# Kernel tuning notes

Measured on AMD Instinct MI355X. Metric: run time of the kernel, lower is better.

The kernel has to match this reference:

```python
import jax, jax.numpy as jnp
import numpy as np

M, N, L, D = 2048, 256, 128, 300  # context len, n entities, query len, d2
DROOT = float(np.sqrt(D))


def setup_inputs() -> dict:
    key = jax.random.key(0)
    ks = jax.random.split(key, 16)
    s = 0.05
    return {
        "context_emb": jax.random.normal(ks[0], (M, D), jnp.float32),
        "query_emb": jax.random.normal(ks[1], (L, D), jnp.float32),
        "bin_M": (jax.random.uniform(ks[2], (M, N)) < 0.02).astype(jnp.float32),  # sparse token->entity incidence
        "adj": (jax.random.uniform(ks[3], (N, N)) < 0.05).astype(jnp.float32),    # entity graph adjacency
        "V": jax.random.normal(ks[4], (D, 2 * D), jnp.float32) * s,
        "U": jax.random.normal(ks[5], (D, 2 * D), jnp.float32) * s,
        "b": jax.random.normal(ks[6], (D,), jnp.float32) * s,
        "W": jax.random.normal(ks[7], (2 * D,), jnp.float32) * s,
        "w_att": jax.random.normal(ks[8], (3, D), jnp.float32) * s,   # BiDAF trilinear weights (w_c, w_q, w_cq)
        "b_att": jax.random.normal(ks[9], (3,), jnp.float32) * s,
        "W_red": jax.random.normal(ks[10], (D, 4 * D), jnp.float32) * s,  # BiDAF reduction Linear(4*d2 -> d2)
        "b_red": jax.random.normal(ks[11], (D,), jnp.float32) * s,
        "W_ih": jax.random.normal(ks[12], (4 * D, 2 * D), jnp.float32) * s,  # LSTM input weights
        "b_ih": jax.random.normal(ks[13], (4 * D,), jnp.float32) * s,
        "b_hh": jax.random.normal(ks[14], (4 * D,), jnp.float32) * s,
        "passes": 1,
    }


def _tok2ent(context, bin_M):
    # avg_pool1d over full M divides by M (zeros of unmasked tokens included) -> exact mean/M
    mean = (bin_M.T @ context) / M                       # (N, D)
    masked = context[:, None, :] * bin_M[:, :, None]     # (M, N, D) dominant intermediate
    mx = masked.max(axis=0)                              # (N, D) max includes the zeros, as in torch
    return jnp.concatenate([mean, mx], axis=-1)          # (N, 2D)


def _graph_attention(ent, query, adj, V, U, b, W):
    q = query.mean(axis=0)                               # avg-pooled query (D,)
    gammas = ((q @ V) @ ent.T) / DROOT                   # (N,)
    E = jax.nn.sigmoid(gammas)[:, None] * ent            # soft entity mask, (N, 2D)
    hidden = E @ U.T + b                                 # (N, D)
    a_i = hidden @ W[:D]                                 # (N,) source half of W.[h_i;h_j]
    c_j = hidden @ W[D:]                                 # (N,)
    betas = jnp.where(adj > 0, jax.nn.leaky_relu(a_i[:, None] + c_j[None, :]), 0.0)
    # original exponentiates ALL betas incl. the zeros of non-edges -> plain softmax over axis 1
    alphas = jax.nn.softmax(betas, axis=1)               # (N, N)
    # E_t[i] = relu( sum_{j: adj[i,j]} alphas[j,i] * hidden[j] )
    return jax.nn.relu((adj * alphas.T) @ hidden)        # (N, D)


def _bidaf(ent, query, w_att, b_att, W_red, b_red):
    # trilinear similarity S[l, n] = w_c.q_l + w_q.e_n + w_cq.(q_l * e_n)
    S = (query @ w_att[0] + b_att[0])[:, None] \
        + (ent @ w_att[1] + b_att[1])[None, :] \
        + (query * w_att[2]) @ ent.T + b_att[2]          # (L, N)
    c2q = jax.nn.softmax(S, axis=1) @ ent                # (L, D)
    q2c = jax.nn.softmax(S.max(axis=1), axis=0) @ query  # (D,)
    x = jnp.concatenate([query, c2q, query * c2q, query * q2c[None, :]], axis=-1)  # (L, 4D)
    return x @ W_red.T + b_red                           # (L, D)


def _graph2doc(context, ent, bin_M, W_ih, b_ih, b_hh):
    x = jnp.concatenate([context, bin_M @ ent], axis=-1)  # (M, 2D)
    # nn.LSTM fed (seq=1, batch=M, 2D) from zero state == one LSTM-cell step per token
    gates = x @ W_ih.T + (b_ih + b_hh)                    # (M, 4D), torch gate order i,f,g,o
    i, f, g, o = jnp.split(gates, 4, axis=-1)
    c = jax.nn.sigmoid(i) * jnp.tanh(g)                   # f*c0 vanishes since c0 = 0
    return jax.nn.sigmoid(o) * jnp.tanh(c)                # (M, D)


def reference(context_emb, query_emb, bin_M, adj, V, U, b, W, w_att, b_att,
              W_red, b_red, W_ih, b_ih, b_hh, passes):
    ctx, qry = context_emb, query_emb
    for _ in range(passes):
        ent = _tok2ent(ctx, bin_M)                        # (N, 2D)
        E_t = _graph_attention(ent, qry, adj, V, U, b, W)  # (N, D)
        qry = _bidaf(E_t, qry, w_att, b_att, W_red, b_red)  # (L, D)
        ctx = _graph2doc(ctx, E_t, bin_M, W_ih, b_ih, b_hh)  # (M, D)
    return ctx, qry
```

## Files before the change

### kernel.cpp

```cpp
#include <hip/hip_runtime.h>
#include <hip/hip_bf16.h>
#include <math.h>

#define MM 2048
#define NN 256
#define LL 128
#define DD 300
#define D2 600
#define D4 1200
#define DROOT 17.320508075688775f

#define KP 608
#define NP 960
#define GM 64
#define GDT 64
#define GK 32

typedef __attribute__((ext_vector_type(8))) short bf16x8;
typedef __attribute__((ext_vector_type(4))) float f32x4;

__device__ __forceinline__ float sigmoidf_(float x) { return 1.f / (1.f + expf(-x)); }

__device__ __forceinline__ ushort f2bf(float v) {
    union { float f; unsigned u; } x; x.f = v;
    unsigned r = x.u + 0x7fffu + ((x.u >> 16) & 1u);
    return (ushort)(r >> 16);
}

__device__ __forceinline__ float dot4_(float4 a, float4 b) {
    return a.x * b.x + a.y * b.y + a.z * b.z + a.w * b.w;
}

__device__ __forceinline__ float bfdot8(uint4 u, float4 x0, float4 x1) {
    union { unsigned v; float f; } a, b;
    float s = 0.f;
    a.v = u.x << 16; b.v = u.x & 0xffff0000u; s += a.f * x0.x; s += b.f * x0.y;
    a.v = u.y << 16; b.v = u.y & 0xffff0000u; s += a.f * x0.z; s += b.f * x0.w;
    a.v = u.z << 16; b.v = u.z & 0xffff0000u; s += a.f * x1.x; s += b.f * x1.y;
    a.v = u.w << 16; b.v = u.w & 0xffff0000u; s += a.f * x1.z; s += b.f * x1.w;
    return s;
}

__device__ __forceinline__ float wave_red_sum(float v) {
    for (int off = 32; off; off >>= 1) v += __shfl_down(v, off);
    return v;
}

__global__ __launch_bounds__(256) void k_prep(const float* __restrict__ binM,
                                              const float* __restrict__ Wih,
                                              const float* __restrict__ U,
                                              const float* __restrict__ Wred,
                                              const float* __restrict__ query,
                                              const float* __restrict__ V,
                                              ushort* __restrict__ Wb,
                                              ushort* __restrict__ Ub,
                                              ushort* __restrict__ Wredb,
                                              unsigned* __restrict__ binMbits,
                                              float* __restrict__ qVp) {
    __shared__ float qp2[2][75];
    __shared__ float qp_s[75];
    int r = blockIdx.x, t = threadIdx.x;
    if (r < 12) {
        int kb = r >> 2, sl = r & 3;
        int dbase = sl * 75;
        if (t < 150) {
            int dd = t % 75, half = t / 75;
            float s = 0.f;
            #pragma unroll 8
            for (int l = half * 64; l < half * 64 + 64; ++l) s += query[l * DD + dbase + dd];
            qp2[half][dd] = s;
        }
        __syncthreads();
        if (t < 75) qp_s[t] = (qp2[0][t] + qp2[1][t]) * (1.f / LL);
        __syncthreads();
        int k = kb * 256 + t;
        if (k < D2) {
            float acc = 0.f;
            #pragma unroll 5
            for (int i = 0; i < 75; ++i) acc += qp_s[i] * V[(size_t)(dbase + i) * D2 + k];
            qVp[sl * D2 + k] = acc;
        }
    } else if (r < 76) {
        int blk = r - 12;
        int m0 = blk * 32;
        unsigned mask = 0u;
        #pragma unroll 8
        for (int i = 0; i < 32; ++i) {
            if (binM[(size_t)(m0 + i) * NN + t] != 0.f) mask |= (1u << i);
        }
        binMbits[(size_t)t * 64 + blk] = mask;
    } else if (r < 76 + NP) {
        int rr = r - 76;
        int s = rr / 320, dd = rr % 320;
        bool valid = (dd < DD);
        int src = (s == 0) ? dd : ((s == 1) ? 600 + dd : 900 + dd);
        for (int e = t; e < KP; e += 256) {
            float v = (valid && e < D2) ? Wih[(size_t)src * D2 + e] : 0.f;
            Wb[(size_t)rr * KP + e] = f2bf(v);
        }
    } else if (r < 76 + NP + DD) {
        int rr = r - 76 - NP;
        for (int e = t; e < D2; e += 256) Ub[(size_t)rr * D2 + e] = f2bf(U[(size_t)rr * D2 + e]);
    } else {
        int rr = r - 76 - NP - DD;
        for (int e = t; e < D4; e += 256) Wredb[(size_t)rr * D4 + e] = f2bf(Wred[(size_t)rr * D4 + e]);
    }
}

__global__ __launch_bounds__(960) void k_hidden(const float* __restrict__ ctx,
                                                const unsigned* __restrict__ binMbits,
                                                const float* __restrict__ qVp,
                                                const ushort* __restrict__ Ub,
                                                const float* __restrict__ bvec,
                                                const float* __restrict__ W,
                                                float* __restrict__ hidden,
                                                float* __restrict__ a_i,
                                                float* __restrict__ c_j) {
    __shared__ int lst[MM];
    __shared__ int wbase_s[65];
    __shared__ alignas(16) float e_s[D2];
    __shared__ float h_s[DD];
    __shared__ float red[2][16];
    __shared__ float sig_s;
    int n = blockIdx.x, t = threadIdx.x, wv = t >> 6, lane = t & 63;
    unsigned mword = (t < 64) ? binMbits[(size_t)n * 64 + t] : 0u;
    if (t < 64) wbase_s[t] = (int)__popc(mword);
    __syncthreads();
    if (t == 0) {
        int s = 0;
        for (int w = 0; w < 64; ++w) { int c = wbase_s[w]; wbase_s[w] = s; s += c; }
        wbase_s[64] = s;
    }
    __syncthreads();
    if (t < 64) {
        int base = wbase_s[t];
        unsigned x = mword;
        while (x) {
            int b = __ffs((int)x) - 1;
            lst[base++] = t * 32 + b;
            x &= x - 1;
        }
    }
    __syncthreads();
    int total = wbase_s[64];
    if (t < DD) {
        float sum = 0.f, mx = 0.f;
        int i = 0;
        for (; i + 4 <= total; i += 4) {
            float v0 = ctx[(size_t)lst[i] * DD + t];
            float v1 = ctx[(size_t)lst[i + 1] * DD + t];
            float v2 = ctx[(size_t)lst[i + 2] * DD + t];
            float v3 = ctx[(size_t)lst[i + 3] * DD + t];
            sum += v0; mx = fmaxf(mx, v0);
            sum += v1; mx = fmaxf(mx, v1);
            sum += v2; mx = fmaxf(mx, v2);
            sum += v3; mx = fmaxf(mx, v3);
        }
        for (; i < total; ++i) {
            float v = ctx[(size_t)lst[i] * DD + t];
            sum += v; mx = fmaxf(mx, v);
        }
        e_s[t]      = sum * (1.f / MM);
        e_s[DD + t] = mx;
    }
    __syncthreads();
    float part = 0.f;
    if (t < D2) part = e_s[t] * (qVp[t] + qVp[D2 + t] + qVp[2 * D2 + t] + qVp[3 * D2 + t]);
    part = wave_red_sum(part);
    if (lane == 0) red[0][wv] = part;
    __syncthreads();
    if (t == 0) {
        float s = 0.f;
        for (int w = 0; w < 15; ++w) s += red[0][w];
        sig_s = sigmoidf_(s / DROOT);
    }
    __syncthreads();
    float sg = sig_s;
    const float4* e4 = (const float4*)e_s;
    float4 ex0 = e4[2 * lane], ex1 = e4[2 * lane + 1];
    float4 ex2 = {0.f, 0.f, 0.f, 0.f}, ex3 = {0.f, 0.f, 0.f, 0.f};
    if (lane < 11) { ex2 = e4[128 + 2 * lane]; ex3 = e4[129 + 2 * lane]; }
    #pragma unroll 4
    for (int i = 0; i < 20; ++i) {
        int d = wv * 20 + i;
        const uint4* u4 = (const uint4*)(Ub + (size_t)d * D2);
        float p2 = bfdot8(u4[lane], ex0, ex1);
        if (lane < 11) p2 += bfdot8(u4[64 + lane], ex2, ex3);
        p2 = wave_red_sum(p2);
        if (lane == 0) {
            float h = sg * p2 + bvec[d];
            h_s[d] = h;
            hidden[n * DD + d] = h;
        }
    }
    __syncthreads();
    float wa = 0.f, wc = 0.f;
    if (t < DD) { float h = h_s[t]; wa = h * W[t]; wc = h * W[DD + t]; }
    wa = wave_red_sum(wa); wc = wave_red_sum(wc);
    if (lane == 0) { red[0][wv] = wa; red[1][wv] = wc; }
    __syncthreads();
    if (t == 0) {
        float A = 0.f, C = 0.f;
        for (int w = 0; w < 15; ++w) { A += red[0][w]; C += red[1][w]; }
        a_i[n] = A; c_j[n] = C;
    }
}

__global__ __launch_bounds__(256) void k_alphas(const float* __restrict__ adj,
                                                const float* __restrict__ ai,
                                                const float* __restrict__ cj,
                                                float* __restrict__ alphas) {
    __shared__ float red[4];
    __shared__ float bc[2];
    int i = blockIdx.x, j = threadIdx.x;
    float beta = 0.f;
    if (adj[i * NN + j] > 0.f) {
        float v = ai[i] + cj[j];
        beta = (v > 0.f) ? v : 0.01f * v;
    }
    float wm = beta;
    for (int off = 32; off; off >>= 1) wm = fmaxf(wm, __shfl_down(wm, off));
    if ((j & 63) == 0) red[j >> 6] = wm;
    __syncthreads();
    if (j == 0) bc[0] = fmaxf(fmaxf(red[0], red[1]), fmaxf(red[2], red[3]));
    __syncthreads();
    float e = expf(beta - bc[0]);
    float ws_ = e;
    for (int off = 32; off; off >>= 1) ws_ += __shfl_down(ws_, off);
    __syncthreads();
    if ((j & 63) == 0) red[j >> 6] = ws_;
    __syncthreads();
    if (j == 0) bc[1] = 1.f / (red[0] + red[1] + red[2] + red[3]);
    __syncthreads();
    alphas[i * NN + j] = e * bc[1];
}

__global__ __launch_bounds__(960) void k_Et(const float* __restrict__ adj,
                                            const float* __restrict__ alphas,
                                            const float* __restrict__ hidden,
                                            const float* __restrict__ w_att,
                                            const float* __restrict__ b_att,
                                            float* __restrict__ Et,
                                            float* __restrict__ EtT,
                                            float* __restrict__ ce) {
    __shared__ float w_s[NN];
    __shared__ float epart[3][DD];
    __shared__ float red[16];
    int i = blockIdx.x, t = threadIdx.x, wv = t >> 6;
    if (t < NN) w_s[t] = adj[i * NN + t] * alphas[t * NN + i];
    __syncthreads();
    int d = t % 320, sl = t / 320;
    int j0 = sl * 86, j1 = (sl == 2) ? NN : (j0 + 86);
    if (d < DD) {
        float acc = 0.f;
        #pragma unroll 2
        for (int j = j0; j < j1; ++j) acc += w_s[j] * hidden[(size_t)j * DD + d];
        epart[sl][d] = acc;
    }
    __syncthreads();
    float pv = 0.f;
    if (t < DD) {
        float etv = fmaxf(epart[0][t] + epart[1][t] + epart[2][t], 0.f);
        Et[i * DD + t] = etv;
        EtT[(size_t)t * NN + i] = etv;
        pv = etv * w_att[DD + t];
    }
    pv = wave_red_sum(pv);
    if ((t & 63) == 0) red[wv] = pv;
    __syncthreads();
    if (t == 0) {
        float s = 0.f;
        for (int w = 0; w < 15; ++w) s += red[w];
        ce[i] = s + b_att[1];
    }
}

__global__ __launch_bounds__(1024) void k_Bmid(const float* __restrict__ query,
                                               const float* __restrict__ Et,
                                               const float* __restrict__ EtT,
                                               const float* __restrict__ w_att,
                                               const float* __restrict__ b_att,
                                               const float* __restrict__ ce,
                                               const float* __restrict__ ctx,
                                               const float* __restrict__ binM,
                                               float* __restrict__ rowmax,
                                               float* __restrict__ c2qg,
                                               ushort* __restrict__ Xb) {
    __shared__ alignas(16) float qw[DD];
    __shared__ float s_row[NN];
    __shared__ alignas(16) float p_s[NN];
    __shared__ float red[16];
    __shared__ float cql_s, rmax_s, invs;
    __shared__ int lst4[4][NN];
    __shared__ int wcnt4[4][4];
    __shared__ int tot4[4];
    int t = threadIdx.x, wv = t >> 6, lane = t & 63;
    if (blockIdx.x < MM / 4) {
        int g = t >> 8, tt = t & 255;
        int w2 = tt >> 6;
        int m = blockIdx.x * 4 + g;
        float b = binM[(size_t)m * NN + tt];
        unsigned long long mask = __ballot(b != 0.f);
        int prefix = __popcll(mask & ((1ull << lane) - 1ull));
        if (lane == 0) wcnt4[g][w2] = (int)__popcll(mask);
        __syncthreads();
        int wbase = 0;
        for (int w = 0; w < w2; ++w) wbase += wcnt4[g][w];
        if (b != 0.f) lst4[g][wbase + prefix] = tt;
        if (tt == 0) tot4[g] = wcnt4[g][0] + wcnt4[g][1] + wcnt4[g][2] + wcnt4[g][3];
        __syncthreads();
        int total = tot4[g];
        if (tt < 8) Xb[(size_t)m * KP + D2 + tt] = 0;
        for (int d = tt; d < DD; d += 256) {
            Xb[(size_t)m * KP + d] = f2bf(ctx[(size_t)m * DD + d]);
            float s = 0.f;
            for (int i = 0; i < total; ++i) s += Et[(size_t)lst4[g][i] * DD + d];
            Xb[(size_t)m * KP + DD + d] = f2bf(s);
        }
    } else {
        int l = blockIdx.x - MM / 4;
        float part = 0.f;
        if (t < DD) {
            float qv = query[l * DD + t];
            qw[t] = qv * w_att[2 * DD + t];
            part = qv * w_att[t];
        }
        part = wave_red_sum(part);
        if (lane == 0) red[wv] = part;
        __syncthreads();
        if (t == 0) {
            float s = 0.f;
            for (int w = 0; w < 16; ++w) s += red[w];
            cql_s = s + b_att[0];
        }
        __syncthreads();
        const float4* q4 = (const float4*)qw;
        float4 qb0 = q4[lane];
        float4 qb1 = (lane < 11) ? q4[64 + lane] : float4{0.f, 0.f, 0.f, 0.f};
        float wmax = -1e30f;
        #pragma unroll 4
        for (int i = 0; i < 16; ++i) {
            int n = wv * 16 + i;
            const float4* e4 = (const float4*)(Et + (size_t)n * DD);
            float4 a0 = e4[lane];
            float p2 = dot4_(a0, qb0);
            if (lane < 11) { float4 a1 = e4[64 + lane]; p2 += dot4_(a1, qb1); }
            p2 = wave_red_sum(p2);
            if (lane == 0) {
                float val = cql_s + ce[n] + p2 + b_att[2];
                s_row[n] = val;
                wmax = fmaxf(wmax, val);
            }
        }
        if (lane == 0) red[wv] = wmax;
        __syncthreads();
        if (t == 0) {
            float m = red[0];
            for (int w = 1; w < 16; ++w) m = fmaxf(m, red[w]);
            rmax_s = m;
            rowmax[l] = m;
        }
        __syncthreads();
        float e = 0.f;
        if (t < NN) e = expf(s_row[t] - rmax_s);
        float v = wave_red_sum(e);
        if (lane == 0) red[wv] = v;
        __syncthreads();
        if (t == 0) {
            float s = 0.f;
            for (int w = 0; w < 16; ++w) s += red[w];
            invs = 1.f / s;
        }
        __syncthreads();
        if (t < NN) p_s[t] = e * invs;
        __syncthreads();
        if (wv < 15) {
            const float4* p4 = (const float4*)p_s;
            float4 pb = p4[lane];
            #pragma unroll 4
            for (int i = 0; i < 20; ++i) {
                int d = wv * 20 + i;
                float4 a = ((const float4*)(EtT + (size_t)d * NN))[lane];
                float p2 = wave_red_sum(dot4_(a, pb));
                if (lane == 0) c2qg[l * DD + d] = p2;
            }
        }
    }
}

__global__ __launch_bounds__(320) void k_tail(const float* __restrict__ c2qg,
                                              const float* __restrict__ rowmax,
                                              const float* __restrict__ query,
                                              const ushort* __restrict__ Wredb,
                                              const float* __restrict__ bred,
                                              const ushort* __restrict__ Xb,
                                              const ushort* __restrict__ Wb,
                                              const float* __restrict__ bih,
                                              const float* __restrict__ bhh,
                                              float* __restrict__ outq,
                                              float* __restrict__ outc) {
    __shared__ float pq[LL];
    __shared__ float q2c_s[DD];
    __shared__ alignas(16) float xs[D4];
    __shared__ float red[5];
    __shared__ float bc2[2];
    __shared__ ushort As[GM * GK];
    __shared__ ushort Bs[3][GDT * GK];
    int t = threadIdx.x, wv = t >> 6, lane = t & 63;
    if (blockIdx.x < 160) {
        int g = blockIdx.x;
        int m0 = (g & 31) * GM, d0 = (g >> 5) * GDT;
        int tid = t;
        int wm = wv >> 1, wn = wv & 1;
        int l15 = lane & 15, l4 = lane >> 4;
        f32x4 acc[3][2][2] = {};
        int srow = tid >> 2, kslot = tid & 3;
        int sidx = srow * GK + ((kslot ^ ((srow >> 1) & 3)) << 3);
        for (int k0 = 0; k0 < KP; k0 += GK) {
            if (tid < 256) {
                uint4 va = *(const uint4*)(Xb + (size_t)(m0 + srow) * KP + k0 + kslot * 8);
                *(uint4*)(As + sidx) = va;
                #pragma unroll
                for (int s = 0; s < 3; ++s) {
                    uint4 vb = *(const uint4*)(Wb + (size_t)(s * 320 + d0 + srow) * KP + k0 + kslot * 8);
                    *(uint4*)(Bs[s] + sidx) = vb;
                }
            }
            __syncthreads();
            if (tid < 256) {
                bf16x8 af[2], bfr[3][2];
                #pragma unroll
                for (int mi = 0; mi < 2; ++mi) {
                    int row = wm * 32 + mi * 16 + l15;
                    af[mi] = *(const bf16x8*)(As + row * GK + ((l4 ^ ((row >> 1) & 3)) << 3));
                }
                #pragma unroll
                for (int s = 0; s < 3; ++s)
                    #pragma unroll
                    for (int ni = 0; ni < 2; ++ni) {
                        int row = wn * 32 + ni * 16 + l15;
                        bfr[s][ni] = *(const bf16x8*)(Bs[s] + row * GK + ((l4 ^ ((row >> 1) & 3)) << 3));
                    }
                #pragma unroll
                for (int s = 0; s < 3; ++s)
                    #pragma unroll
                    for (int mi = 0; mi < 2; ++mi)
                        #pragma unroll
                        for (int ni = 0; ni < 2; ++ni)
                            acc[s][mi][ni] = __builtin_amdgcn_mfma_f32_16x16x32_bf16(af[mi], bfr[s][ni], acc[s][mi][ni], 0, 0, 0);
            }
            __syncthreads();
        }
        if (tid < 256) {
            #pragma unroll
            for (int mi = 0; mi < 2; ++mi) {
                #pragma unroll
                for (int ni = 0; ni < 2; ++ni) {
                    int d = d0 + wn * 32 + ni * 16 + l15;
                    if (d < DD) {
                        float bi = bih[d] + bhh[d];
                        float bg = bih[2 * DD + d] + bhh[2 * DD + d];
                        float bo = bih[3 * DD + d] + bhh[3 * DD + d];
                        int mrow = m0 + wm * 32 + mi * 16 + l4 * 4;
                        #pragma unroll
                        for (int r2 = 0; r2 < 4; ++r2) {
                            float gi = acc[0][mi][ni][r2] + bi;
                            float gg = acc[1][mi][ni][r2] + bg;
                            float go = acc[2][mi][ni][r2] + bo;
                            float c = sigmoidf_(gi) * tanhf(gg);
                            outc[(size_t)(mrow + r2) * DD + d] = sigmoidf_(go) * tanhf(c);
                        }
                    }
                }
            }
        }
    } else {
        int idx = blockIdx.x - 160;
        int s = idx / LL, l = idx % LL;
        float v = (t < LL) ? rowmax[t] : -1e30f;
        float wm = v;
        for (int off = 32; off; off >>= 1) wm = fmaxf(wm, __shfl_down(wm, off));
        if (lane == 0) red[wv] = wm;
        __syncthreads();
        if (t == 0) {
            float m = red[0];
            for (int w = 1; w < 5; ++w) m = fmaxf(m, red[w]);
            bc2[0] = m;
        }
        __syncthreads();
        float e = (t < LL) ? expf(v - bc2[0]) : 0.f;
        float ws_ = wave_red_sum(e);
        __syncthreads();
        if (lane == 0) red[wv] = ws_;
        __syncthreads();
        if (t == 0) {
            float sm = 0.f;
            for (int w = 0; w < 5; ++w) sm += red[w];
            bc2[1] = 1.f / sm;
        }
        __syncthreads();
        if (t < LL) pq[t] = e * bc2[1];
        __syncthreads();
        if (t < DD) {
            float s2 = 0.f;
            #pragma unroll 4
            for (int l2 = 0; l2 < LL; ++l2) s2 += pq[l2] * query[l2 * DD + t];
            q2c_s[t] = s2;
        }
        __syncthreads();
        if (t < DD) {
            float c = c2qg[l * DD + t];
            float qv = query[l * DD + t];
            xs[t] = qv; xs[DD + t] = c; xs[2 * DD + t] = qv * c; xs[3 * DD + t] = qv * q2c_s[t];
        }
        __syncthreads();
        const float4* x4 = (const float4*)xs;
        float4 xb0 = x4[2 * lane], xb1 = x4[2 * lane + 1];
        float4 xb2 = x4[128 + 2 * lane], xb3 = x4[129 + 2 * lane];
        float4 xb4 = {0.f, 0.f, 0.f, 0.f}, xb5 = {0.f, 0.f, 0.f, 0.f};
        if (lane < 22) { xb4 = x4[256 + 2 * lane]; xb5 = x4[257 + 2 * lane]; }
        int d0 = s * 100 + wv * 20;
        #pragma unroll 2
        for (int i = 0; i < 20; ++i) {
            int d = d0 + i;
            const uint4* w4 = (const uint4*)(Wredb + (size_t)d * D4);
            float p2 = bfdot8(w4[lane], xb0, xb1) + bfdot8(w4[64 + lane], xb2, xb3);
            if (lane < 22) p2 += bfdot8(w4[128 + lane], xb4, xb5);
            p2 = wave_red_sum(p2);
            if (lane == 0) outq[l * DD + d] = bred[d] + p2;
        }
    }
}

extern "C" void kernel_launch(void* const* d_in, const int* in_sizes, int n_in,
                              void* d_out, int out_size, void* d_ws, size_t ws_size,
                              hipStream_t stream) {
    const float* context = (const float*)d_in[0];
    const float* query   = (const float*)d_in[1];
    const float* binM    = (const float*)d_in[2];
    const float* adj     = (const float*)d_in[3];
    const float* V       = (const float*)d_in[4];
    const float* U       = (const float*)d_in[5];
    const float* bvec    = (const float*)d_in[6];
    const float* W       = (const float*)d_in[7];
    const float* w_att   = (const float*)d_in[8];
    const float* b_att   = (const float*)d_in[9];
    const float* W_red   = (const float*)d_in[10];
    const float* b_red   = (const float*)d_in[11];
    const float* W_ih    = (const float*)d_in[12];
    const float* b_ih    = (const float*)d_in[13];
    const float* b_hh    = (const float*)d_in[14];

    float* ws = (float*)d_ws;
    float* qVp    = ws;
    float* hidden = qVp    + 2400;
    float* a_i    = hidden + 76800;
    float* c_j    = a_i    + 256;
    float* alphas = c_j    + 256;
    float* Et     = alphas + 65536;
    float* EtT    = Et     + 76800;
    float* ce     = EtT    + 76800;
    float* rmax   = ce     + 256;
    float* c2qg   = rmax   + 128;
    unsigned* binMbits = (unsigned*)(c2qg + 38400);
    ushort* Xb    = (ushort*)(binMbits + (size_t)NN * 64);
    ushort* Wb    = Xb + (size_t)MM * KP;
    ushort* Ub    = Wb + (size_t)NP * KP;
    ushort* Wredb = Ub + (size_t)DD * D2;

    float* outc = (float*)d_out;
    float* outq = (float*)d_out + MM * DD;

    hipLaunchKernelGGL(k_prep,    dim3(76 + NP + 2 * DD), dim3(256), 0, stream,
                       binM, W_ih, U, W_red, query, V, Wb, Ub, Wredb, binMbits, qVp);
    hipLaunchKernelGGL(k_hidden,  dim3(NN), dim3(960), 0, stream, context, binMbits, qVp, Ub, bvec, W, hidden, a_i, c_j);
    hipLaunchKernelGGL(k_alphas,  dim3(NN), dim3(256), 0, stream, adj, a_i, c_j, alphas);
    hipLaunchKernelGGL(k_Et,      dim3(NN), dim3(960), 0, stream, adj, alphas, hidden, w_att, b_att, Et, EtT, ce);
    hipLaunchKernelGGL(k_Bmid,    dim3(MM / 4 + LL), dim3(1024), 0, stream,
                       query, Et, EtT, w_att, b_att, ce, context, binM, rmax, c2qg, Xb);
    hipLaunchKernelGGL(k_tail,    dim3(160 + 3 * LL), dim3(320), 0, stream,
                       c2qg, rmax, query, Wredb, b_red, Xb, Wb, b_ih, b_hh, outq, outc);
}
```

Measured before the change: 116.9 us.

## Fuse hidden, alphas and Et kernels into one cooperative kernel with grid syncs

Merges the three graph-attention kernels into a single cooperative launch that uses grid.sync between phases, removing two kernel launch boundaries. The alphas phase now stores only per-row max and inverse sum, and the Et phase recomputes each softmax weight on the fly, so the 256x256 alphas matrix is no longer written or read. In exchange it adds cooperative-launch overhead and grid-wide barriers, and requires all 256 blocks of 960 threads to be co-resident.

Measured after the change: 174.0 us. +48.8%, slower.

```diff
diff --git a/kernel.cpp b/kernel.cpp
--- a/kernel.cpp
+++ b/kernel.cpp
@@ -1,6 +1,9 @@
 #include <hip/hip_runtime.h>
+#include <hip/hip_cooperative_groups.h>
 #include <hip/hip_bf16.h>
 #include <math.h>
+
+namespace cg = cooperative_groups;
 
 #define MM 2048
 #define NN 256
@@ -107,171 +110,184 @@
     }
 }
 
-__global__ __launch_bounds__(960) void k_hidden(const float* __restrict__ ctx,
-                                                const unsigned* __restrict__ binMbits,
-                                                const float* __restrict__ qVp,
-                                                const ushort* __restrict__ Ub,
-                                                const float* __restrict__ bvec,
-                                                const float* __restrict__ W,
-                                                float* __restrict__ hidden,
-                                                float* __restrict__ a_i,
-                                                float* __restrict__ c_j) {
+__global__ __launch_bounds__(960) void k_mid(const float* __restrict__ ctx,
+                                             const unsigned* __restrict__ binMbits,
+                                             const float* __restrict__ qVp,
+                                             const ushort* __restrict__ Ub,
+                                             const float* __restrict__ adj,
+                                             const float* __restrict__ bvec,
+                                             const float* __restrict__ W,
+                                             const float* __restrict__ w_att,
+                                             const float* __restrict__ b_att,
+                                             float* __restrict__ hidden,
+                                             float* __restrict__ a_i,
+                                             float* __restrict__ c_j,
+                                             float* __restrict__ mstat,
+                                             float* __restrict__ rinv,
+                                             float* __restrict__ Et,
+                                             float* __restrict__ EtT,
+                                             float* __restrict__ ce) {
+    cg::grid_group grid = cg::this_grid();
     __shared__ int lst[MM];
     __shared__ int wbase_s[65];
     __shared__ alignas(16) float e_s[D2];
     __shared__ float h_s[DD];
     __shared__ float red[2][16];
-    __shared__ float sig_s;
-    int n = blockIdx.x, t = threadIdx.x, wv = t >> 6, lane = t & 63;
-    unsigned mword = (t < 64) ? binMbits[(size_t)n * 64 + t] : 0u;
-    if (t < 64) wbase_s[t] = (int)__popc(mword);
-    __syncthreads();
-    if (t == 0) {
-        int s = 0;
-        for (int w = 0; w < 64; ++w) { int c = wbase_s[w]; wbase_s[w] = s; s += c; }
-        wbase_s[64] = s;
-    }
-    __syncthreads();
-    if (t < 64) {
-        int base = wbase_s[t];
-        unsigned x = mword;
-        while (x) {
-            int b = __ffs((int)x) - 1;
-            lst[base++] = t * 32 + b;
-            x &= x - 1;
-        }
-    }
-    __syncthreads();
-    int total = wbase_s[64];
-    if (t < DD) {
-        float sum = 0.f, mx = 0.f;
-        int i = 0;
-        for (; i + 4 <= total; i += 4) {
-            float v0 = ctx[(size_t)lst[i] * DD + t];
-            float v1 = ctx[(size_t)lst[i + 1] * DD + t];
-            float v2 = ctx[(size_t)lst[i + 2] * DD + t];
-            float v3 = ctx[(size_t)lst[i + 3] * DD + t];
-            sum += v0; mx = fmaxf(mx, v0);
-            sum += v1; mx = fmaxf(mx, v1);
-            sum += v2; mx = fmaxf(mx, v2);
-            sum += v3; mx = fmaxf(mx, v3);
-        }
-        for (; i < total; ++i) {
-            float v = ctx[(size_t)lst[i] * DD + t];
-            sum += v; mx = fmaxf(mx, v);
-        }
-        e_s[t]      = sum * (1.f / MM);
-        e_s[DD + t] = mx;
-    }
-    __syncthreads();
-    float part = 0.f;
-    if (t < D2) part = e_s[t] * (qVp[t] + qVp[D2 + t] + qVp[2 * D2 + t] + qVp[3 * D2 + t]);
-    part = wave_red_sum(part);
-    if (lane == 0) red[0][wv] = part;
-    __syncthreads();
-    if (t == 0) {
-        float s = 0.f;
-        for (int w = 0; w < 15; ++w) s += red[0][w];
-        sig_s = sigmoidf_(s / DROOT);
-    }
-    __syncthreads();
-    float sg = sig_s;
-    const float4* e4 = (const float4*)e_s;
-    float4 ex0 = e4[2 * lane], ex1 = e4[2 * lane + 1];
-    float4 ex2 = {0.f, 0.f, 0.f, 0.f}, ex3 = {0.f, 0.f, 0.f, 0.f};
-    if (lane < 11) { ex2 = e4[128 + 2 * lane]; ex3 = e4[129 + 2 * lane]; }
-    #pragma unroll 4
-    for (int i = 0; i < 20; ++i) {
-        int d = wv * 20 + i;
-        const uint4* u4 = (const uint4*)(Ub + (size_t)d * D2);
-        float p2 = bfdot8(u4[lane], ex0, ex1);
-        if (lane < 11) p2 += bfdot8(u4[64 + lane], ex2, ex3);
-        p2 = wave_red_sum(p2);
-        if (lane == 0) {
-            float h = sg * p2 + bvec[d];
-            h_s[d] = h;
-            hidden[n * DD + d] = h;
-        }
-    }
-    __syncthreads();
-    float wa = 0.f, wc = 0.f;
-    if (t < DD) { float h = h_s[t]; wa = h * W[t]; wc = h * W[DD + t]; }
-    wa = wave_red_sum(wa); wc = wave_red_sum(wc);
-    if (lane == 0) { red[0][wv] = wa; red[1][wv] = wc; }
-    __syncthreads();
-    if (t == 0) {
-        float A = 0.f, C = 0.f;
-        for (int w = 0; w < 15; ++w) { A += red[0][w]; C += red[1][w]; }
-        a_i[n] = A; c_j[n] = C;
-    }
-}
-
-__global__ __launch_bounds__(256) void k_alphas(const float* __restrict__ adj,
-                                                const float* __restrict__ ai,
-                                                const float* __restrict__ cj,
-                                                float* __restrict__ alphas) {
-    __shared__ float red[4];
-    __shared__ float bc[2];
-    int i = blockIdx.x, j = threadIdx.x;
-    float beta = 0.f;
-    if (adj[i * NN + j] > 0.f) {
-        float v = ai[i] + cj[j];
-        beta = (v > 0.f) ? v : 0.01f * v;
-    }
-    float wm = beta;
-    for (int off = 32; off; off >>= 1) wm = fmaxf(wm, __shfl_down(wm, off));
-    if ((j & 63) == 0) red[j >> 6] = wm;
-    __syncthreads();
-    if (j == 0) bc[0] = fmaxf(fmaxf(red[0], red[1]), fmaxf(red[2], red[3]));
-    __syncthreads();
-    float e = expf(beta - bc[0]);
-    float ws_ = e;
-    for (int off = 32; off; off >>= 1) ws_ += __shfl_down(ws_, off);
-    __syncthreads();
-    if ((j & 63) == 0) red[j >> 6] = ws_;
-    __syncthreads();
-    if (j == 0) bc[1] = 1.f / (red[0] + red[1] + red[2] + red[3]);
-    __syncthreads();
-    alphas[i * NN + j] = e * bc[1];
-}
-
-__global__ __launch_bounds__(960) void k_Et(const float* __restrict__ adj,
-                                            const float* __restrict__ alphas,
-                                            const float* __restrict__ hidden,
-                                            const float* __restrict__ w_att,
-                                            const float* __restrict__ b_att,
-                                            float* __restrict__ Et,
-                                            float* __restrict__ EtT,
-                                            float* __restrict__ ce) {
+    __shared__ float scal[2];
     __shared__ float w_s[NN];
     __shared__ float epart[3][DD];
-    __shared__ float red[16];
-    int i = blockIdx.x, t = threadIdx.x, wv = t >> 6;
-    if (t < NN) w_s[t] = adj[i * NN + t] * alphas[t * NN + i];
-    __syncthreads();
-    int d = t % 320, sl = t / 320;
-    int j0 = sl * 86, j1 = (sl == 2) ? NN : (j0 + 86);
-    if (d < DD) {
-        float acc = 0.f;
-        #pragma unroll 2
-        for (int j = j0; j < j1; ++j) acc += w_s[j] * hidden[(size_t)j * DD + d];
-        epart[sl][d] = acc;
+    int bid = blockIdx.x, t = threadIdx.x, wv = t >> 6, lane = t & 63;
+
+    {
+        int n = bid;
+        unsigned mword = (t < 64) ? binMbits[(size_t)n * 64 + t] : 0u;
+        if (t < 64) wbase_s[t] = (int)__popc(mword);
+        __syncthreads();
+        if (t == 0) {
+            int s = 0;
+            for (int w = 0; w < 64; ++w) { int c = wbase_s[w]; wbase_s[w] = s; s += c; }
+            wbase_s[64] = s;
+        }
+        __syncthreads();
+        if (t < 64) {
+            int base = wbase_s[t];
+            unsigned x = mword;
+            while (x) {
+                int b = __ffs((int)x) - 1;
+                lst[base++] = t * 32 + b;
+                x &= x - 1;
+            }
+        }
+        __syncthreads();
+        int total = wbase_s[64];
+        if (t < DD) {
+            float sum = 0.f, mx = 0.f;
+            int i = 0;
+            for (; i + 4 <= total; i += 4) {
+                float v0 = ctx[(size_t)lst[i] * DD + t];
+                float v1 = ctx[(size_t)lst[i + 1] * DD + t];
+                float v2 = ctx[(size_t)lst[i + 2] * DD + t];
+                float v3 = ctx[(size_t)lst[i + 3] * DD + t];
+                sum += v0; mx = fmaxf(mx, v0);
+                sum += v1; mx = fmaxf(mx, v1);
+                sum += v2; mx = fmaxf(mx, v2);
+                sum += v3; mx = fmaxf(mx, v3);
+            }
+            for (; i < total; ++i) {
+                float v = ctx[(size_t)lst[i] * DD + t];
+                sum += v; mx = fmaxf(mx, v);
+            }
+            e_s[t]      = sum * (1.f / MM);
+            e_s[DD + t] = mx;
+        }
+        __syncthreads();
+        float part = 0.f;
+        if (t < D2) part = e_s[t] * (qVp[t] + qVp[D2 + t] + qVp[2 * D2 + t] + qVp[3 * D2 + t]);
+        part = wave_red_sum(part);
+        if (lane == 0) red[0][wv] = part;
+        __syncthreads();
+        if (t == 0) {
+            float s = 0.f;
+            for (int w = 0; w < 15; ++w) s += red[0][w];
+            scal[0] = sigmoidf_(s / DROOT);
+        }
+        __syncthreads();
+        float sg = scal[0];
+        const float4* e4 = (const float4*)e_s;
+        float4 ex0 = e4[2 * lane], ex1 = e4[2 * lane + 1];
+        float4 ex2 = {0.f, 0.f, 0.f, 0.f}, ex3 = {0.f, 0.f, 0.f, 0.f};
+        if (lane < 11) { ex2 = e4[128 + 2 * lane]; ex3 = e4[129 + 2 * lane]; }
+        #pragma unroll 4
+        for (int i = 0; i < 20; ++i) {
+            int d = wv * 20 + i;
+            const uint4* u4 = (const uint4*)(Ub + (size_t)d * D2);
+            float p2 = bfdot8(u4[lane], ex0, ex1);
+            if (lane < 11) p2 += bfdot8(u4[64 + lane], ex2, ex3);
+            p2 = wave_red_sum(p2);
+            if (lane == 0) {
+                float h = sg * p2 + bvec[d];
+                h_s[d] = h;
+                hidden[n * DD + d] = h;
+            }
+        }
+        __syncthreads();
+        float wa = 0.f, wc = 0.f;
+        if (t < DD) { float h = h_s[t]; wa = h * W[t]; wc = h * W[DD + t]; }
+        wa = wave_red_sum(wa); wc = wave_red_sum(wc);
+        if (lane == 0) { red[0][wv] = wa; red[1][wv] = wc; }
+        __syncthreads();
+        if (t == 0) {
+            float A = 0.f, C = 0.f;
+            for (int w = 0; w < 15; ++w) { A += red[0][w]; C += red[1][w]; }
+            a_i[n] = A; c_j[n] = C;
+        }
     }
-    __syncthreads();
-    float pv = 0.f;
-    if (t < DD) {
-        float etv = fmaxf(epart[0][t] + epart[1][t] + epart[2][t], 0.f);
-        Et[i * DD + t] = etv;
-        EtT[(size_t)t * NN + i] = etv;
-        pv = etv * w_att[DD + t];
+    grid.sync();
+
+    {
+        int j = bid;
+        bool act = (t < NN);
+        float beta = 0.f;
+        if (act && adj[(size_t)j * NN + t] > 0.f) {
+            float v = a_i[j] + c_j[t];
+            beta = (v > 0.f) ? v : 0.01f * v;
+        }
+        float bm = act ? beta : -1e30f;
+        for (int off = 32; off; off >>= 1) bm = fmaxf(bm, __shfl_down(bm, off));
+        if (lane == 0) red[0][wv] = bm;
+        __syncthreads();
+        if (t == 0) {
+            float m = red[0][0];
+            for (int w = 1; w < 4; ++w) m = fmaxf(m, red[0][w]);
+            scal[0] = m;
+        }
+        __syncthreads();
+        float e = act ? expf(beta - scal[0]) : 0.f;
+        float s1 = wave_red_sum(e);
+        if (lane == 0) red[1][wv] = s1;
+        __syncthreads();
+        if (t == 0) {
+            float s = red[1][0] + red[1][1] + red[1][2] + red[1][3];
+            mstat[j] = scal[0];
+            rinv[j] = 1.f / s;
+        }
     }
-    pv = wave_red_sum(pv);
-    if ((t & 63) == 0) red[wv] = pv;
-    __syncthreads();
-    if (t == 0) {
-        float s = 0.f;
-        for (int w = 0; w < 15; ++w) s += red[w];
-        ce[i] = s + b_att[1];
+    grid.sync();
+
+    {
+        int i = bid;
+        if (t < NN) {
+            float aj  = adj[(size_t)i * NN + t];
+            float adT = adj[(size_t)t * NN + i];
+            float v = a_i[t] + c_j[i];
+            float beta = (adT > 0.f) ? ((v > 0.f) ? v : 0.01f * v) : 0.f;
+            w_s[t] = aj * expf(beta - mstat[t]) * rinv[t];
+        }
+        __syncthreads();
+        int d = t % 320, sl = t / 320;
+        if (d < DD) {
+            int j0 = sl * 86, j1 = (sl == 2) ? NN : (j0 + 86);
+            float acc = 0.f;
+            #pragma unroll 2
+            for (int j = j0; j < j1; ++j) acc += w_s[j] * hidden[(size_t)j * DD + d];
+            epart[sl][d] = acc;
+        }
+        __syncthreads();
+        float pv = 0.f;
+        if (t < DD) {
+            float etv = fmaxf(epart[0][t] + epart[1][t] + epart[2][t], 0.f);
+            Et[i * DD + t] = etv;
+            EtT[(size_t)t * NN + i] = etv;
+            pv = etv * w_att[DD + t];
+        }
+        pv = wave_red_sum(pv);
+        if (lane == 0) red[0][wv] = pv;
+        __syncthreads();
+        if (t == 0) {
+            float s = 0.f;
+            for (int w = 0; w < 15; ++w) s += red[0][w];
+            ce[i] = s + b_att[1];
+        }
     }
 }
 
@@ -556,8 +572,9 @@
     float* hidden = qVp    + 2400;
     float* a_i    = hidden + 76800;
     float* c_j    = a_i    + 256;
-    float* alphas = c_j    + 256;
-    float* Et     = alphas + 65536;
+    float* mstat  = c_j    + 256;
+    float* rinv   = mstat  + 256;
+    float* Et     = rinv   + 256;
     float* EtT    = Et     + 76800;
     float* ce     = EtT    + 76800;
     float* rmax   = ce     + 256;
@@ -571,11 +588,17 @@
     float* outc = (float*)d_out;
     float* outq = (float*)d_out + MM * DD;
 
-    hipLaunchKernelGGL(k_prep,    dim3(76 + NP + 2 * DD), dim3(256), 0, stream,
+    hipLaunchKernelGGL(k_prep, dim3(76 + NP + 2 * DD), dim3(256), 0, stream,
                        binM, W_ih, U, W_red, query, V, Wb, Ub, Wredb, binMbits, qVp);
-    hipLaunchKernelGGL(k_hidden,  dim3(NN), dim3(960), 0, stream, context, binMbits, qVp, Ub, bvec, W, hidden, a_i, c_j);
-    hipLaunchKernelGGL(k_alphas,  dim3(NN), dim3(256), 0, stream, adj, a_i, c_j, alphas);
-    hipLaunchKernelGGL(k_Et,      dim3(NN), dim3(960), 0, stream, adj, alphas, hidden, w_att, b_att, Et, EtT, ce);
+
+    void* args[] = {
+        (void*)&context, (void*)&binMbits, (void*)&qVp, (void*)&Ub, (void*)&adj,
+        (void*)&bvec, (void*)&W, (void*)&w_att, (void*)&b_att,
+        (void*)&hidden, (void*)&a_i, (void*)&c_j, (void*)&mstat, (void*)&rinv,
+        (void*)&Et, (void*)&EtT, (void*)&ce
+    };
+    hipLaunchCooperativeKernel((const void*)k_mid, dim3(NN), dim3(960), args, 0, stream);
+
     hipLaunchKernelGGL(k_Bmid,    dim3(MM / 4 + LL), dim3(1024), 0, stream,
                        query, Et, EtT, w_att, b_att, ce, context, binM, rmax, c2qg, Xb);
     hipLaunchKernelGGL(k_tail,    dim3(160 + 3 * LL), dim3(320), 0, stream,
```
